# Performance work log

Measured on AMD Instinct MI355X. Metric: run time of the kernel, lower is better.

Reference implementation:

```python
import jax, jax.numpy as jnp
import numpy as np

EMB_DIM = 2048
USER_DIM = 256
NUM_EXPERTS = 64
TOP_K = 8
N_TOKENS = 16384


def setup_inputs() -> dict:
    key = jax.random.key(0)
    k_h, k_u, k_w = jax.random.split(key, 3)
    h = jax.random.normal(k_h, (N_TOKENS, EMB_DIM), dtype=jnp.float32)
    u = jax.random.normal(k_u, (N_TOKENS, USER_DIM), dtype=jnp.float32)
    # nn.Linear weight is [out, in]; we store transposed [in, out] for x @ W
    W = jax.random.normal(k_w, (EMB_DIM + USER_DIM, NUM_EXPERTS), dtype=jnp.float32) * (1.0 / np.sqrt(EMB_DIM + USER_DIM))
    b = jnp.zeros((NUM_EXPERTS,), dtype=jnp.float32)
    return {"h": h, "u": u, "W": W, "b": b}


def reference(h, u, W, b):
    # gate logits: [N, E]
    g = jnp.concatenate([h, u], axis=-1) @ W + b
    w = jax.nn.softmax(g, axis=-1)
    # top-k mask + renormalize (top_k < num_experts)
    _, top_idx = jax.lax.top_k(w, TOP_K)                       # [N, k]
    mask = jax.nn.one_hot(top_idx, NUM_EXPERTS, dtype=w.dtype).sum(axis=-2)  # [N, E]
    w = w * mask
    w = w / (w.sum(axis=-1, keepdims=True) + 1e-9)
    return w
```

## Files before the change

### kernel.cpp

```cpp
#include <hip/hip_runtime.h>

#define EMB 2048
#define UDIM 256
#define KTOT 2304
#define NE 64
#define TOPK 8
#define TPB 32
#define LP 65
#define NSTEP (KTOT / 32)
#define SSH 6144

typedef __attribute__((ext_vector_type(8))) short short8;
typedef __attribute__((ext_vector_type(4))) float f32x4;

__device__ __forceinline__ unsigned short bf16h(float x) {
  unsigned uu = __builtin_bit_cast(unsigned, x);
  return (unsigned short)((uu + 0x7FFFu + ((uu >> 16) & 1u)) >> 16);
}
__device__ __forceinline__ float bf2f(unsigned short s) {
  return __builtin_bit_cast(float, ((unsigned)s) << 16);
}

__global__ __launch_bounds__(256)
void prep_w(const float* __restrict__ W, unsigned short* __restrict__ wb) {
  const int flat = blockIdx.x * 256 + threadIdx.x;
  const int k = flat >> 6;
  const int n = flat & 63;
  const float w = W[flat];
  const unsigned short h0 = bf16h(w);
  const float r1 = w - bf2f(h0);
  const unsigned short h1 = bf16h(r1);
  const float r2 = r1 - bf2f(h1);
  const unsigned short h2 = bf16h(r2);

  const int s = k >> 5;
  const int kk = k & 31;
  const int lane = (kk >> 3) * 16 + (n & 15);
  const int j = kk & 7;
  const int nt = n >> 4;
  const size_t base = (size_t)s * SSH + ((size_t)nt * 64 + lane) * 8 + j;
  wb[base] = h0;
  wb[base + 2048] = h1;
  wb[base + 4096] = h2;
}

__global__ __launch_bounds__(512, 4)
void gate_mfma(const float* __restrict__ h, const float* __restrict__ u,
               const unsigned short* __restrict__ wb,
               const float* __restrict__ b, float* __restrict__ out) {
  __shared__ float slab[TPB * LP];

  const int tid = threadIdx.x;
  const int lane = tid & 63;
  const int wid = __builtin_amdgcn_readfirstlane(tid >> 6);
  const int tw = wid & 1;
  const int kq = wid >> 1;
  const int mm = lane & 15;
  const int q8 = (lane >> 4) * 8;
  const int tok0 = blockIdx.x * TPB;
  const int token = tok0 + tw * 16 + mm;

  const float* hrow = h + (size_t)token * EMB + q8;
  const float* urow = u + (size_t)token * UDIM + q8;
  const unsigned short* wlane = wb + (size_t)lane * 8;

  f32x4 acc[4];
#pragma unroll
  for (int nt = 0; nt < 4; ++nt) acc[nt] = 0.f;

  auto run = [&](const float* __restrict__ xp, int kw0, int nsteps) {
    f32x4 c0 = *(const f32x4*)(xp);
    f32x4 c1 = *(const f32x4*)(xp + 4);
    f32x4 n0 = 0.f, n1 = 0.f;
    if (nsteps > 1) {
      n0 = *(const f32x4*)(xp + 32);
      n1 = *(const f32x4*)(xp + 36);
    }
    const int as0 = kw0 >> 5;
    for (int s = 0; s < nsteps; ++s) {
      f32x4 f0 = 0.f, f1 = 0.f;
      if (s + 2 < nsteps) {
        f0 = *(const f32x4*)(xp + (s + 2) * 32);
        f1 = *(const f32x4*)(xp + (s + 2) * 32 + 4);
      }
      const unsigned short* ws = wlane + (size_t)(as0 + s) * SSH;
      short8 Bv[3][4];
#pragma unroll
      for (int p = 0; p < 3; ++p)
#pragma unroll
        for (int nt = 0; nt < 4; ++nt)
          Bv[p][nt] = *(const short8*)(ws + (p * 4 + nt) * 512);

      float xs[8] = {c0[0], c0[1], c0[2], c0[3], c1[0], c1[1], c1[2], c1[3]};
      short8 A0, A1, A2;
#pragma unroll
      for (int j = 0; j < 8; ++j) {
        const unsigned short h0 = bf16h(xs[j]);
        const float r1 = xs[j] - bf2f(h0);
        const unsigned short h1 = bf16h(r1);
        const float r2 = r1 - bf2f(h1);
        A0[j] = (short)h0;
        A1[j] = (short)h1;
        A2[j] = (short)bf16h(r2);
      }
#pragma unroll
      for (int nt = 0; nt < 4; ++nt) {
        acc[nt] = __builtin_amdgcn_mfma_f32_16x16x32_bf16(A0, Bv[0][nt], acc[nt], 0, 0, 0);
        acc[nt] = __builtin_amdgcn_mfma_f32_16x16x32_bf16(A0, Bv[1][nt], acc[nt], 0, 0, 0);
        acc[nt] = __builtin_amdgcn_mfma_f32_16x16x32_bf16(A1, Bv[0][nt], acc[nt], 0, 0, 0);
        acc[nt] = __builtin_amdgcn_mfma_f32_16x16x32_bf16(A1, Bv[1][nt], acc[nt], 0, 0, 0);
        acc[nt] = __builtin_amdgcn_mfma_f32_16x16x32_bf16(A0, Bv[2][nt], acc[nt], 0, 0, 0);
        acc[nt] = __builtin_amdgcn_mfma_f32_16x16x32_bf16(A2, Bv[0][nt], acc[nt], 0, 0, 0);
      }
      c0 = n0; c1 = n1; n0 = f0; n1 = f1;
    }
  };

  const int kw0 = kq * 576;
  if (kq < 3) {
    run(hrow + kw0, kw0, 18);
  } else {
    run(hrow + 1728, 1728, 10);
    run(urow, 2048, 8);
  }

  const int row = tw * 16 + (lane >> 4) * 4;
  for (int ph = 0; ph < 4; ++ph) {
    if (kq == ph) {
#pragma unroll
      for (int nt = 0; nt < 4; ++nt)
#pragma unroll
        for (int r = 0; r < 4; ++r) {
          float* p = &slab[(row + r) * LP + nt * 16 + mm];
          if (ph == 0) *p = acc[nt][r]; else *p += acc[nt][r];
        }
    }
    __syncthreads();
  }

  const float bias = b[lane];
#pragma unroll
  for (int tt = 0; tt < 4; ++tt) {
    const int t = wid * 4 + tt;
    float g = slab[t * LP + lane] + bias;

    float m = g;
#pragma unroll
    for (int off = 32; off > 0; off >>= 1)
      m = fmaxf(m, __shfl_xor(m, off));
    float pexp = __expf(g - m);
    float s = pexp;
#pragma unroll
    for (int off = 32; off > 0; off >>= 1)
      s += __shfl_xor(s, off);
    const float pn = pexp / s;

    float vv = pn;
    float topsum = 0.f;
    int sel = 0;
    for (int r = 0; r < TOPK; ++r) {
      float mv = vv;
      int mi = lane;
#pragma unroll
      for (int off = 32; off > 0; off >>= 1) {
        const float ov = __shfl_xor(mv, off);
        const int oi = __shfl_xor(mi, off);
        if (ov > mv || (ov == mv && oi < mi)) { mv = ov; mi = oi; }
      }
      topsum += mv;
      if (lane == mi) { sel = 1; vv = -1.f; }
    }

    out[(size_t)(tok0 + t) * NE + lane] =
        sel ? pn / (topsum + 1e-9f) : 0.f;
  }
}

extern "C" void kernel_launch(void* const* d_in, const int* in_sizes, int n_in,
                              void* d_out, int out_size, void* d_ws, size_t ws_size,
                              hipStream_t stream) {
  const float* h = (const float*)d_in[0];
  const float* u = (const float*)d_in[1];
  const float* W = (const float*)d_in[2];
  const float* b = (const float*)d_in[3];
  float* out = (float*)d_out;

  unsigned short* wb = (unsigned short*)d_ws;

  const int n_tokens = in_sizes[0] / EMB;

  hipLaunchKernelGGL(prep_w, dim3(KTOT * NE / 256), dim3(256), 0, stream, W, wb);
  hipLaunchKernelGGL(gate_mfma, dim3(n_tokens / TPB), dim3(512), 0, stream,
                     h, u, wb, b, out);
}
```

Measured before the change: 262.2 us.

## Halve tokens per block, split K across eight waves, use packed bf16 conversion

Each block now handles 16 tokens with all eight waves splitting the K dimension (288 columns each) instead of two token groups times four K-quarters, and the occupancy hint is raised to 8 blocks. The cross-wave reduction becomes two-phase into four LDS slabs summed at the softmax stage, replacing four serialized phases. The three-way bf16 split now uses the v_cvt_pk_bf16_f32 instruction to convert pairs at once, and the input prefetch distance drops from two steps to one. Trade-offs: the W operand is reloaded per block for half as many tokens, doubling weight traffic relative to tokens processed, and the shorter prefetch may expose more global latency.

```diff
diff --git a/kernel.cpp b/kernel.cpp
--- a/kernel.cpp
+++ b/kernel.cpp
@@ -5,13 +5,13 @@
 #define KTOT 2304
 #define NE 64
 #define TOPK 8
-#define TPB 32
+#define TPB 16
 #define LP 65
-#define NSTEP (KTOT / 32)
 #define SSH 6144
 
 typedef __attribute__((ext_vector_type(8))) short short8;
 typedef __attribute__((ext_vector_type(4))) float f32x4;
+typedef __attribute__((ext_vector_type(4))) unsigned int u32x4;
 
 __device__ __forceinline__ unsigned short bf16h(float x) {
   unsigned uu = __builtin_bit_cast(unsigned, x);
@@ -19,6 +19,12 @@
 }
 __device__ __forceinline__ float bf2f(unsigned short s) {
   return __builtin_bit_cast(float, ((unsigned)s) << 16);
+}
+
+__device__ __forceinline__ unsigned cvtpk(float a, float b) {
+  unsigned r;
+  asm("v_cvt_pk_bf16_f32 %0, %1, %2" : "=v"(r) : "v"(a), "v"(b));
+  return r;
 }
 
 __global__ __launch_bounds__(256)
@@ -44,21 +50,19 @@
   wb[base + 4096] = h2;
 }
 
-__global__ __launch_bounds__(512, 4)
+__global__ __launch_bounds__(512, 8)
 void gate_mfma(const float* __restrict__ h, const float* __restrict__ u,
                const unsigned short* __restrict__ wb,
                const float* __restrict__ b, float* __restrict__ out) {
-  __shared__ float slab[TPB * LP];
+  __shared__ float slab[4][TPB * LP];
 
   const int tid = threadIdx.x;
   const int lane = tid & 63;
-  const int wid = __builtin_amdgcn_readfirstlane(tid >> 6);
-  const int tw = wid & 1;
-  const int kq = wid >> 1;
+  const int kq = __builtin_amdgcn_readfirstlane(tid >> 6);
   const int mm = lane & 15;
   const int q8 = (lane >> 4) * 8;
   const int tok0 = blockIdx.x * TPB;
-  const int token = tok0 + tw * 16 + mm;
+  const int token = tok0 + mm;
 
   const float* hrow = h + (size_t)token * EMB + q8;
   const float* urow = u + (size_t)token * UDIM + q8;
@@ -71,18 +75,8 @@
   auto run = [&](const float* __restrict__ xp, int kw0, int nsteps) {
     f32x4 c0 = *(const f32x4*)(xp);
     f32x4 c1 = *(const f32x4*)(xp + 4);
-    f32x4 n0 = 0.f, n1 = 0.f;
-    if (nsteps > 1) {
-      n0 = *(const f32x4*)(xp + 32);
-      n1 = *(const f32x4*)(xp + 36);
-    }
     const int as0 = kw0 >> 5;
     for (int s = 0; s < nsteps; ++s) {
-      f32x4 f0 = 0.f, f1 = 0.f;
-      if (s + 2 < nsteps) {
-        f0 = *(const f32x4*)(xp + (s + 2) * 32);
-        f1 = *(const f32x4*)(xp + (s + 2) * 32 + 4);
-      }
       const unsigned short* ws = wlane + (size_t)(as0 + s) * SSH;
       short8 Bv[3][4];
 #pragma unroll
@@ -91,18 +85,30 @@
         for (int nt = 0; nt < 4; ++nt)
           Bv[p][nt] = *(const short8*)(ws + (p * 4 + nt) * 512);
 
+      f32x4 n0 = 0.f, n1 = 0.f;
+      if (s + 1 < nsteps) {
+        n0 = *(const f32x4*)(xp + (s + 1) * 32);
+        n1 = *(const f32x4*)(xp + (s + 1) * 32 + 4);
+      }
+
       float xs[8] = {c0[0], c0[1], c0[2], c0[3], c1[0], c1[1], c1[2], c1[3]};
-      short8 A0, A1, A2;
-#pragma unroll
-      for (int j = 0; j < 8; ++j) {
-        const unsigned short h0 = bf16h(xs[j]);
-        const float r1 = xs[j] - bf2f(h0);
-        const unsigned short h1 = bf16h(r1);
-        const float r2 = r1 - bf2f(h1);
-        A0[j] = (short)h0;
-        A1[j] = (short)h1;
-        A2[j] = (short)bf16h(r2);
-      }
+      u32x4 W0, W1, W2;
+#pragma unroll
+      for (int k2 = 0; k2 < 4; ++k2) {
+        const float a = xs[2 * k2], bb = xs[2 * k2 + 1];
+        const unsigned p0 = cvtpk(a, bb);
+        const float a1 = a - __builtin_bit_cast(float, p0 << 16);
+        const float b1 = bb - __builtin_bit_cast(float, p0 & 0xFFFF0000u);
+        const unsigned p1 = cvtpk(a1, b1);
+        const float a2 = a1 - __builtin_bit_cast(float, p1 << 16);
+        const float b2 = b1 - __builtin_bit_cast(float, p1 & 0xFFFF0000u);
+        const unsigned p2 = cvtpk(a2, b2);
+        W0[k2] = p0; W1[k2] = p1; W2[k2] = p2;
+      }
+      const short8 A0 = __builtin_bit_cast(short8, W0);
+      const short8 A1 = __builtin_bit_cast(short8, W1);
+      const short8 A2 = __builtin_bit_cast(short8, W2);
+
 #pragma unroll
       for (int nt = 0; nt < 4; ++nt) {
         acc[nt] = __builtin_amdgcn_mfma_f32_16x16x32_bf16(A0, Bv[0][nt], acc[nt], 0, 0, 0);
@@ -112,37 +118,42 @@
         acc[nt] = __builtin_amdgcn_mfma_f32_16x16x32_bf16(A0, Bv[2][nt], acc[nt], 0, 0, 0);
         acc[nt] = __builtin_amdgcn_mfma_f32_16x16x32_bf16(A2, Bv[0][nt], acc[nt], 0, 0, 0);
       }
-      c0 = n0; c1 = n1; n0 = f0; n1 = f1;
+      c0 = n0; c1 = n1;
     }
   };
 
-  const int kw0 = kq * 576;
-  if (kq < 3) {
-    run(hrow + kw0, kw0, 18);
+  if (kq < 7) {
+    run(hrow + kq * 288, kq * 288, 9);
   } else {
-    run(hrow + 1728, 1728, 10);
+    run(hrow + 2016, 2016, 1);
     run(urow, 2048, 8);
   }
 
-  const int row = tw * 16 + (lane >> 4) * 4;
-  for (int ph = 0; ph < 4; ++ph) {
-    if (kq == ph) {
-#pragma unroll
-      for (int nt = 0; nt < 4; ++nt)
-#pragma unroll
-        for (int r = 0; r < 4; ++r) {
-          float* p = &slab[(row + r) * LP + nt * 16 + mm];
-          if (ph == 0) *p = acc[nt][r]; else *p += acc[nt][r];
-        }
-    }
-    __syncthreads();
-  }
+  const int row = (lane >> 4) * 4;
+  const int bsel = kq & 3;
+  if (kq < 4) {
+#pragma unroll
+    for (int nt = 0; nt < 4; ++nt)
+#pragma unroll
+      for (int r = 0; r < 4; ++r)
+        slab[bsel][(row + r) * LP + nt * 16 + mm] = acc[nt][r];
+  }
+  __syncthreads();
+  if (kq >= 4) {
+#pragma unroll
+    for (int nt = 0; nt < 4; ++nt)
+#pragma unroll
+      for (int r = 0; r < 4; ++r)
+        slab[bsel][(row + r) * LP + nt * 16 + mm] += acc[nt][r];
+  }
+  __syncthreads();
 
   const float bias = b[lane];
 #pragma unroll
-  for (int tt = 0; tt < 4; ++tt) {
-    const int t = wid * 4 + tt;
-    float g = slab[t * LP + lane] + bias;
+  for (int tt = 0; tt < 2; ++tt) {
+    const int t = kq * 2 + tt;
+    float g = slab[0][t * LP + lane] + slab[1][t * LP + lane] +
+              slab[2][t * LP + lane] + slab[3][t * LP + lane] + bias;
 
     float m = g;
 #pragma unroll
```

After: 265.1 us. Within noise of the previous version (+1.1%).
